# Kernel tuning notes

Hardware: AMD Instinct MI355X
Metric: run time of the kernel (lower is better)

## Reference

```python
import jax, jax.numpy as jnp
import numpy as np

B, S, E = 2, 1024, 768
H, D = 12, 64          # num_heads, head_dim
M = 768                # mlp_hidden_size
Q = 4                  # q_stride
EPS = 1e-5


def _layernorm(x, w, b):
    mu = x.mean(-1, keepdims=True)
    var = ((x - mu) ** 2).mean(-1, keepdims=True)
    return (x - mu) * jax.lax.rsqrt(var + EPS) * w + b


def setup_inputs() -> dict:
    key = jax.random.key(0)
    ks = jax.random.split(key, 16)
    s = 0.02
    d = {
        'x': jax.random.normal(ks[0], (B, S, E), jnp.float32),
        'ln1_w': jnp.ones((E,), jnp.float32), 'ln1_b': jnp.zeros((E,), jnp.float32),
        'Wq': jax.random.normal(ks[1], (E, E), jnp.float32) * s, 'bq': jnp.zeros((E,), jnp.float32),
        'Wk': jax.random.normal(ks[2], (E, E), jnp.float32) * s, 'bk': jnp.zeros((E,), jnp.float32),
        'Wv': jax.random.normal(ks[3], (E, E), jnp.float32) * s, 'bv': jnp.zeros((E,), jnp.float32),
        'Wo': jax.random.normal(ks[4], (E, E), jnp.float32) * s, 'bo': jnp.zeros((E,), jnp.float32),
        'pond': jnp.zeros((), jnp.float32),  # ponderation_param
        'ln2_w': jnp.ones((E,), jnp.float32), 'ln2_b': jnp.zeros((E,), jnp.float32),
        'fc1_W': jax.random.normal(ks[5], (Q * M, E), jnp.float32) * s, 'fc1_b': jnp.zeros((Q * M,), jnp.float32),
        'vqc_W': jax.random.normal(ks[6], (M, M), jnp.float32) * s, 'vqc_b': jnp.zeros((M,), jnp.float32),
        'fc2_W': jax.random.normal(ks[7], (E, Q * M), jnp.float32) * s, 'fc2_b': jnp.zeros((E,), jnp.float32),
    }
    return d


def reference(x, ln1_w, ln1_b, Wq, bq, Wk, bk, Wv, bv, Wo, bo, pond,
              ln2_w, ln2_b, fc1_W, fc1_b, vqc_W, vqc_b, fc2_W, fc2_b):
    # --- attention sublayer ---
    h = _layernorm(x, ln1_w, ln1_b)
    def heads(W, b):
        return (h @ W.T + b).reshape(B, S, H, D).transpose(0, 2, 1, 3)  # [B,H,S,D]
    q, k, v = heads(Wq, bq), heads(Wk, bk), heads(Wv, bv)

    # N=2: einsum with identity A reduces to q k^T
    logits = jnp.einsum('bhid,bhjd->bhij', q, k) / jnp.sqrt(jnp.float32(D))
    attn = jax.nn.softmax(logits, axis=-1)  # dropout is identity at inference

    # RBF similarity blending ('linear' ponderation)
    q_norm = (q ** 2).sum(-1, keepdims=True)                  # [B,H,S,1]
    k_norm = (k ** 2).sum(-1, keepdims=True).swapaxes(-2, -1)  # [B,H,1,S]
    d2 = jnp.maximum(q_norm + k_norm - 2.0 * jnp.einsum('bhid,bhjd->bhij', q, k), 0.0)
    sigma2 = jnp.clip(q_norm, 1e-8, 1e4)
    rbf = jnp.exp(-d2 / sigma2)
    rbf = rbf / jnp.maximum(rbf.sum(-1, keepdims=True), 1e-8)
    rbf = jnp.nan_to_num(rbf, nan=0.0, posinf=0.0, neginf=0.0)
    s_val = jax.nn.sigmoid(pond)
    p0, p1 = 1.0 - s_val, s_val
    attn = (p0 * attn + p1 * rbf) / (p0 + p1 + 1e-7)

    vals = jnp.einsum('bhij,bhjd->bhid', attn, v)
    vals = vals.transpose(0, 2, 1, 3).reshape(B, S, E)
    x = x + (vals @ Wo.T + bo)

    # --- sliced MLP sublayer (q_stride=4, overlapping offset-1 slices) ---
    y = _layernorm(x, ln2_w, ln2_b)
    h1 = y @ fc1_W.T + fc1_b                                  # [B,S,Q*M]
    slices = jnp.stack([h1[:, :, i:i + M] for i in range(Q)], axis=2)  # [B,S,Q,M]
    z = slices @ vqc_W.T + vqc_b                              # vqc (linear fallback)
    z = z.transpose(0, 1, 3, 2).reshape(B, S, Q * M)          # permute(0,1,3,2).view
    z = jax.nn.gelu(z, approximate=False)
    out = z @ fc2_W.T + fc2_b
    return x + out
```

## Files before the change

### kernel.cpp

```cpp
#include <hip/hip_runtime.h>
#include <math.h>

#define E_DIM 768
#define S_LEN 1024
#define B_SZ 2
#define H_CNT 12
#define D_HEAD 64
#define M_DIM 768
#define Q_STRIDE 4
#define N_FC1 771

typedef __attribute__((ext_vector_type(8))) short bf16x8;
typedef __attribute__((ext_vector_type(4))) float f32x4;

#define AS1 __attribute__((address_space(1)))
#define AS3 __attribute__((address_space(3)))

__device__ __forceinline__ void gld_lds16(void* lds, const void* g) {
    __builtin_amdgcn_global_load_lds((const AS1 void*)g, (AS3 void*)lds, 16, 0, 0);
}

__device__ __forceinline__ short f2bf(float f) {
    unsigned u = __float_as_uint(f);
    unsigned r = (u + 0x7fffu + ((u >> 16) & 1u)) >> 16;
    return (short)r;
}

__device__ __forceinline__ float bf2f(short s) {
    return __uint_as_float(((unsigned)(unsigned short)s) << 16);
}


__device__ __forceinline__ float block_reduce_sum(float v, volatile float* red) {
#pragma unroll
    for (int off = 32; off > 0; off >>= 1) v += __shfl_xor(v, off);
    __syncthreads();
    if ((threadIdx.x & 63) == 0) red[threadIdx.x >> 6] = v;
    __syncthreads();
    return red[0] + red[1] + red[2] + red[3];
}


__global__ __launch_bounds__(256) void preamble(
        const float* __restrict__ Wq, const float* __restrict__ Wk,
        const float* __restrict__ Wv, const float* __restrict__ Wo,
        const float* __restrict__ fc1W, const float* __restrict__ vqcW,
        const float* __restrict__ fc2W, short* __restrict__ dst,
        const float* __restrict__ bq, const float* __restrict__ bk,
        const float* __restrict__ bv, float* __restrict__ bqkv,
        const float* __restrict__ x, const float* __restrict__ ln1_w,
        const float* __restrict__ ln1_b, short* __restrict__ actb) {
    __shared__ float red[4];
    int tid = threadIdx.x;
    if (blockIdx.x < 2048) {
        int row = blockIdx.x;
        const float* xr = x + (size_t)row * E_DIM;
        float v0 = xr[tid], v1 = xr[tid + 256], v2 = xr[tid + 512];
        float s = block_reduce_sum(v0 + v1 + v2, red);
        float mu = s * (1.0f / E_DIM);
        float d0 = v0 - mu, d1 = v1 - mu, d2 = v2 - mu;
        float var = block_reduce_sum(d0 * d0 + d1 * d1 + d2 * d2, red) * (1.0f / E_DIM);
        float rs = rsqrtf(var + 1e-5f);
        short* orow = actb + (size_t)row * E_DIM;
        orow[tid]       = f2bf(d0 * rs * ln1_w[tid]       + ln1_b[tid]);
        orow[tid + 256] = f2bf(d1 * rs * ln1_w[tid + 256] + ln1_b[tid + 256]);
        orow[tid + 512] = f2bf(d2 * rs * ln1_w[tid + 512] + ln1_b[tid + 512]);
        return;
    }
    if (blockIdx.x == 2048) {
#pragma unroll
        for (int u = 0; u < 9; u++) {
            int i = tid + u * 256;
            float v = (i < 768) ? bq[i] : (i < 1536) ? bk[i - 768] : bv[i - 1536];
            bqkv[i] = v;
        }
        return;
    }
    int t = (blockIdx.x - 2049) * 256 + tid;
    if (t >= 1475136) return;
    int e = t * 4;
    const float* src; int off;
    if      (e < 589824)  { src = Wq;   off = e; }
    else if (e < 1179648) { src = Wk;   off = e - 589824; }
    else if (e < 1769472) { src = Wv;   off = e - 1179648; }
    else if (e < 2359296) { src = Wo;   off = e - 1769472; }
    else if (e < 2951424) { src = fc1W; off = e - 2359296; }
    else if (e < 3541248) { src = vqcW; off = e - 2951424; }
    else                  { src = fc2W; off = e - 3541248; }
    float4 v = *(const float4*)(src + off);
    short4 o = make_short4(f2bf(v.x), f2bf(v.y), f2bf(v.z), f2bf(v.w));
    *(short4*)(dst + e) = o;
}


template <int OUTMODE, int MR>
__global__ __launch_bounds__(256, 2) void gemm_bf16(
        const short* __restrict__ A, int lda,
        const short* __restrict__ W, int ldw,
        const float* __restrict__ bias,
        void* __restrict__ outp, int ldo, size_t spitch,
        short* __restrict__ Kfp, short* __restrict__ Vfp,
        int N, int klen, int dogelu) {
    constexpr int MI = MR / 32;
    constexpr int AH = MR * 32;
    constexpr int NA = MR / 64;
    constexpr int ASL = 2 * AH;
    __shared__ short At[2 * ASL];
    __shared__ short Bt[2 * 8192];
    const int tid = threadIdx.x;
    const int lane = tid & 63;
    const int wave = tid >> 6;
    const int wr = (wave >> 1) * (MI * 16);
    const int wc = (wave & 1) * 64;
    const int ml = lane & 15;
    const int kq = lane >> 4;
    const int row0 = blockIdx.y * MR;
    const int col0 = blockIdx.x * 128;
    const int kbase = blockIdx.z * klen;

    const short* Ag[NA]; int aoff[NA];
#pragma unroll
    for (int u = 0; u < NA; u++) {
        int c = tid + u * 256;
        int am = c >> 2, ak = ((c & 3) ^ ((am >> 1) & 3)) * 8;
        Ag[u] = A + (size_t)(row0 + am) * lda + ak + kbase;
        aoff[u] = c * 8;
    }
    const int c0 = tid, c1 = tid + 256;
    const int bm0 = c0 >> 2, bk0 = (((c0 & 3) ^ ((bm0 >> 1) & 3))) * 8;
    const int bm1 = c1 >> 2, bk1 = (((c1 & 3) ^ ((bm1 >> 1) & 3))) * 8;
    int wrow0 = col0 + bm0; if (wrow0 > N - 1) wrow0 = N - 1;
    int wrow1 = col0 + bm1; if (wrow1 > N - 1) wrow1 = N - 1;
    const short* Wg0 = W + (size_t)wrow0 * ldw + bk0 + kbase;
    const short* Wg1 = W + (size_t)wrow1 * ldw + bk1 + kbase;

    const int kxor = (kq ^ ((ml >> 1) & 3)) * 8;

    f32x4 acc[MI][4];
#pragma unroll
    for (int i = 0; i < MI; i++)
#pragma unroll
        for (int j = 0; j < 4; j++) acc[i][j] = {0.f, 0.f, 0.f, 0.f};

    auto stage = [&](int buf, int k0) {
        short* Ab = At + buf * ASL;
        short* Bb = Bt + buf * 8192;
#pragma unroll
        for (int u = 0; u < NA; u++) {
            gld_lds16(Ab + aoff[u], Ag[u] + k0);
            gld_lds16(Ab + AH + aoff[u], Ag[u] + k0 + 32);
        }
        gld_lds16(Bb + c0 * 8, Wg0 + k0);
        gld_lds16(Bb + c1 * 8, Wg1 + k0);
        gld_lds16(Bb + 4096 + c0 * 8, Wg0 + k0 + 32);
        gld_lds16(Bb + 4096 + c1 * 8, Wg1 + k0 + 32);
    };

    stage(0, 0);
    int cur = 0;
    for (int k0 = 0; k0 < klen; k0 += 64) {
        __syncthreads();
        if (k0 + 64 < klen) stage(cur ^ 1, k0 + 64);
        const short* Ac = At + cur * ASL;
        const short* Bc = Bt + cur * 8192;
#pragma unroll
        for (int half = 0; half < 2; half++) {
            const short* Ah = Ac + half * AH;
            const short* Bh = Bc + half * 4096;
            bf16x8 af[MI], bfr[4];
#pragma unroll
            for (int i = 0; i < MI; i++)
                af[i] = *(const bf16x8*)&Ah[(wr + i * 16 + ml) * 32 + kxor];
#pragma unroll
            for (int j = 0; j < 4; j++)
                bfr[j] = *(const bf16x8*)&Bh[(wc + j * 16 + ml) * 32 + kxor];
#pragma unroll
            for (int i = 0; i < MI; i++)
#pragma unroll
                for (int j = 0; j < 4; j++)
                    acc[i][j] = __builtin_amdgcn_mfma_f32_16x16x32_bf16(af[i], bfr[j], acc[i][j], 0, 0, 0);
        }
        cur ^= 1;
    }

#pragma unroll
    for (int i = 0; i < MI; i++) {
#pragma unroll
        for (int j = 0; j < 4; j++) {
#pragma unroll
            for (int rr = 0; rr < 4; rr++) {
                int r = row0 + wr + i * 16 + kq * 4 + rr;
                int c = col0 + wc + j * 16 + ml;
                if (c < N) {
                    float v = acc[i][j][rr];
                    if (OUTMODE < 4) v += bias[c];
                    if (OUTMODE == 2 && dogelu)
                        v = 0.5f * v * (1.0f + erff(v * 0.70710678118654752f));
                    if (OUTMODE == 2) {
                        ((short*)outp)[(size_t)(r >> 2) * ldo + c * 4 + (r & 3)] = f2bf(v);
                    } else if (OUTMODE == 5) {
                        ((short*)outp)[blockIdx.z * spitch + (size_t)r * ldo + c] = f2bf(v);
                    } else if (OUTMODE == 3) {
                        int s = r & 1023, bb = r >> 10;
                        if (c < 768) {
                            ((short*)outp)[(size_t)r * 768 + c] = f2bf(v);
                        } else if (c < 1536) {
                            int df = c - 768; int hh = df >> 6, d = df & 63;
                            int bh2 = bb * 12 + hh;
                            size_t idx = ((size_t)(bh2 * 64 + (s >> 4)) * 2 + (d >> 5)) * 512
                                       + (size_t)((d >> 3) & 3) * 128 + (size_t)(s & 15) * 8 + (d & 7);
                            Kfp[idx] = f2bf(v);
                        } else {
                            int df = c - 1536; int hh = df >> 6, d = df & 63;
                            int bh2 = bb * 12 + hh;
                            size_t idx = ((size_t)(bh2 * 32 + (s >> 5))) * 2048
                                       + (size_t)(d >> 4) * 512 + (size_t)((s >> 3) & 3) * 128
                                       + (size_t)(d & 15) * 8 + (s & 7);
                            Vfp[idx] = f2bf(v);
                        }
                    }
                }
            }
        }
    }
}


__global__ __launch_bounds__(256) void reduce_wo_ln(
        const short* __restrict__ part, const float* __restrict__ bo,
        const float* __restrict__ x, const float* __restrict__ w,
        const float* __restrict__ bvec, float* __restrict__ x2,
        short* __restrict__ y) {
    __shared__ float red[4];
    int row = blockIdx.x, tid = threadIdx.x;
    const size_t SP = (size_t)2048 * 768;
    const short* pr = part + (size_t)row * 768;
    const float* xr = x + (size_t)row * 768;
    float* x2r = x2 + (size_t)row * 768;
    float v[3];
#pragma unroll
    for (int u = 0; u < 3; u++) {
        int c = tid + u * 256;
        float s = bo[c] + xr[c];
#pragma unroll
        for (int z = 0; z < 4; z++) s += bf2f(pr[z * SP + c]);
        v[u] = s; x2r[c] = s;
    }
    float s = block_reduce_sum(v[0] + v[1] + v[2], red);
    float mu = s * (1.0f / 768.f);
    float d0 = v[0] - mu, d1 = v[1] - mu, d2 = v[2] - mu;
    float var = block_reduce_sum(d0 * d0 + d1 * d1 + d2 * d2, red) * (1.0f / 768.f);
    float rs = rsqrtf(var + 1e-5f);
    short* orow = y + (size_t)row * 768;
    orow[tid]       = f2bf(d0 * rs * w[tid]       + bvec[tid]);
    orow[tid + 256] = f2bf(d1 * rs * w[tid + 256] + bvec[tid + 256]);
    orow[tid + 512] = f2bf(d2 * rs * w[tid + 512] + bvec[tid + 512]);
}

__global__ __launch_bounds__(256) void reduce_fc1_expand(
        const short* __restrict__ part, const float* __restrict__ b,
        const short* __restrict__ y, const short* __restrict__ w768,
        short* __restrict__ Avqc) {
    __shared__ float row[772];
    __shared__ float red[4];
    int r = blockIdx.x, tid = threadIdx.x;
    const size_t SP = (size_t)2048 * 768;
    const short* pr = part + (size_t)r * 768;
#pragma unroll
    for (int u = 0; u < 3; u++) {
        int c = tid + u * 256;
        float s = b[c];
#pragma unroll
        for (int z = 0; z < 4; z++) s += bf2f(pr[z * SP + c]);
        row[c] = s;
    }
    const short* yr = y + (size_t)r * 768;
    float y0 = bf2f(yr[tid]), y1 = bf2f(yr[tid + 256]), y2 = bf2f(yr[tid + 512]);
#pragma unroll
    for (int k = 0; k < 3; k++) {
        const short* wk = w768 + k * 768;
        float s = y0 * bf2f(wk[tid]) + y1 * bf2f(wk[tid + 256]) + y2 * bf2f(wk[tid + 512]);
        s = block_reduce_sum(s, red);
        if (tid == 0) row[768 + k] = s + b[768 + k];
    }
    __syncthreads();
#pragma unroll
    for (int q = 0; q < 4; q++) {
        short* orow = Avqc + (size_t)(r * 4 + q) * 768;
#pragma unroll
        for (int u = 0; u < 3; u++) {
            int m = tid + u * 256;
            orow[m] = f2bf(row[m + q]);
        }
    }
}

__global__ __launch_bounds__(256) void reduce_fc2(
        const short* __restrict__ part, const float* __restrict__ b,
        const float* __restrict__ x2, float* __restrict__ out) {
    int t = blockIdx.x * 256 + threadIdx.x;
    int row = t / 192;
    int c = (t - row * 192) * 4;
    size_t off = (size_t)row * 768 + c;
    const size_t SP = (size_t)2048 * 768;
    float4 bb = *(const float4*)(b + c);
    float4 xx = *(const float4*)(x2 + off);
    float o0 = bb.x + xx.x, o1 = bb.y + xx.y, o2 = bb.z + xx.z, o3 = bb.w + xx.w;
#pragma unroll
    for (int z = 0; z < 4; z++) {
        short4 v = *(const short4*)(part + z * SP + off);
        o0 += bf2f(v.x); o1 += bf2f(v.y); o2 += bf2f(v.z); o3 += bf2f(v.w);
    }
    float4 o = make_float4(o0, o1, o2, o3);
    *(float4*)(out + off) = o;
}


__global__ __launch_bounds__(256) void attn_mfma(
        const short* __restrict__ Qb,
        const short* __restrict__ Kf,
        const short* __restrict__ Vf,
        const float* __restrict__ pond,
        short* __restrict__ vals) {
    __shared__ __align__(16) short Kt[2 * 4096];
    __shared__ __align__(16) short Vt[2 * 4096];
    __shared__ float qn_l[4][16];
    __shared__ float is_l[4][16];
    __shared__ float esx[2][16], rsx[2][16];
    __shared__ __align__(16) short Pe[4 * 16 * 72];
    __shared__ __align__(16) short Pr[4 * 16 * 72];

    const int tid = threadIdx.x;
    const int lane = tid & 63;
    const int wave = tid >> 6;
    const int wq = wave & 1;
    const int wp = wave >> 1;
    const int ml = lane & 15;
    const int kq = lane >> 4;
    const int qt2 = blockIdx.x, h = blockIdx.y, b = blockIdx.z;
    const int bh = b * H_CNT + h;

    const int qrow = b * S_LEN + qt2 * 32 + wq * 16 + ml;
    const short* qp = Qb + (size_t)qrow * 768 + h * 64 + kq * 8;
    bf16x8 aq0 = *(const bf16x8*)qp;
    bf16x8 aq1 = *(const bf16x8*)(qp + 32);

    float qn_part = 0.f;
#pragma unroll
    for (int e = 0; e < 8; e++) {
        float v0 = bf2f(aq0[e]), v1 = bf2f(aq1[e]);
        qn_part += v0 * v0 + v1 * v1;
    }
    qn_part += __shfl_xor(qn_part, 16);
    qn_part += __shfl_xor(qn_part, 32);
    if (kq == 0) {
        qn_l[wave][ml] = qn_part;
        float sig = fminf(fmaxf(qn_part, 1e-8f), 1e4f);
        is_l[wave][ml] = 1.0f / sig;
    }
    __syncthreads();

    float qn_r[4], is_r[4];
#pragma unroll
    for (int r = 0; r < 4; r++) {
        qn_r[r] = qn_l[wave][kq * 4 + r];
        is_r[r] = is_l[wave][kq * 4 + r];
    }

    f32x4 Oe[4], Or[4];
#pragma unroll
    for (int dt = 0; dt < 4; dt++) { Oe[dt] = {0.f,0.f,0.f,0.f}; Or[dt] = {0.f,0.f,0.f,0.f}; }
    float es_p[4] = {0.f,0.f,0.f,0.f}, rs_p[4] = {0.f,0.f,0.f,0.f};

    const short* KfB = Kf + (size_t)bh * 65536;
    const short* VfB = Vf + (size_t)bh * 65536;
    short* PeW = Pe + wave * 1152;
    short* PrW = Pr + wave * 1152;
    const short* KtW = Kt + wp * 4096;
    const short* VtW = Vt + wp * 4096;

    for (int it = 0; it < 8; it++) {
        __syncthreads();
        {
            const short* sk0 = KfB + it * 4096 + tid * 8;
            gld_lds16(Kt + tid * 8, sk0);
            gld_lds16(Kt + 2048 + tid * 8, sk0 + 2048);
            const short* sk1 = KfB + (it + 8) * 4096 + tid * 8;
            gld_lds16(Kt + 4096 + tid * 8, sk1);
            gld_lds16(Kt + 6144 + tid * 8, sk1 + 2048);
            const short* sv0 = VfB + it * 4096 + tid * 8;
            gld_lds16(Vt + tid * 8, sv0);
            gld_lds16(Vt + 2048 + tid * 8, sv0 + 2048);
            const short* sv1 = VfB + (it + 8) * 4096 + tid * 8;
            gld_lds16(Vt + 4096 + tid * 8, sv1);
            gld_lds16(Vt + 6144 + tid * 8, sv1 + 2048);
        }
        __syncthreads();

#pragma unroll
        for (int jtl = 0; jtl < 4; jtl++) {
            bf16x8 bk0 = *(const bf16x8*)&KtW[(jtl * 2 + 0) * 512 + lane * 8];
            bf16x8 bk1 = *(const bf16x8*)&KtW[(jtl * 2 + 1) * 512 + lane * 8];
            float knp = 0.f;
#pragma unroll
            for (int e = 0; e < 8; e++) {
                float k0v = bf2f(bk0[e]), k1v = bf2f(bk1[e]);
                knp += k0v * k0v + k1v * k1v;
            }
            knp += __shfl_xor(knp, 16);
            knp += __shfl_xor(knp, 32);
            f32x4 c = {0.f,0.f,0.f,0.f};
            c = __builtin_amdgcn_mfma_f32_16x16x32_bf16(aq0, bk0, c, 0, 0, 0);
            c = __builtin_amdgcn_mfma_f32_16x16x32_bf16(aq1, bk1, c, 0, 0, 0);
#pragma unroll
            for (int r = 0; r < 4; r++) {
                float qk = c[r];
                float e = __expf(qk * 0.125f);
                float tt = (2.f * qk - qn_r[r] - knp) * is_r[r];
                float rb = fminf(__expf(tt), 1.0f);
                es_p[r] += e; rs_p[r] += rb;
                PeW[(kq * 4 + r) * 72 + jtl * 16 + ml] = f2bf(e);
                PrW[(kq * 4 + r) * 72 + jtl * 16 + ml] = f2bf(rb);
            }
        }

#pragma unroll
        for (int jcl = 0; jcl < 2; jcl++) {
            bf16x8 pa_e = *(const bf16x8*)&PeW[ml * 72 + jcl * 32 + kq * 8];
            bf16x8 pa_r = *(const bf16x8*)&PrW[ml * 72 + jcl * 32 + kq * 8];
#pragma unroll
            for (int dt = 0; dt < 4; dt++) {
                bf16x8 bv = *(const bf16x8*)&VtW[(jcl * 4 + dt) * 512 + lane * 8];
                Oe[dt] = __builtin_amdgcn_mfma_f32_16x16x32_bf16(pa_e, bv, Oe[dt], 0, 0, 0);
                Or[dt] = __builtin_amdgcn_mfma_f32_16x16x32_bf16(pa_r, bv, Or[dt], 0, 0, 0);
            }
        }
    }

#pragma unroll
    for (int off = 1; off <= 8; off <<= 1) {
#pragma unroll
        for (int r = 0; r < 4; r++) {
            es_p[r] += __shfl_xor(es_p[r], off);
            rs_p[r] += __shfl_xor(rs_p[r], off);
        }
    }

    __syncthreads();
    float* cb = (float*)Kt;
    if (wp == 1) {
        float* cl = cb + (size_t)(wq * 64 + lane) * 32;
#pragma unroll
        for (int dt = 0; dt < 4; dt++)
#pragma unroll
            for (int r = 0; r < 4; r++) {
                cl[dt * 4 + r] = Oe[dt][r];
                cl[16 + dt * 4 + r] = Or[dt][r];
            }
        if (ml == 0) {
#pragma unroll
            for (int r = 0; r < 4; r++) {
                esx[wq][kq * 4 + r] = es_p[r];
                rsx[wq][kq * 4 + r] = rs_p[r];
            }
        }
    }
    __syncthreads();
    if (wp == 0) {
        float p = pond[0];
        float sv = 1.0f / (1.0f + __expf(-p));
        float p0 = 1.0f - sv, p1 = sv;
        float blendinv = 1.0f / (p0 + p1 + 1e-7f);
        const float* cl = cb + (size_t)(wq * 64 + lane) * 32;
        float we[4], wr[4];
#pragma unroll
        for (int r = 0; r < 4; r++) {
            float es = es_p[r] + esx[wq][kq * 4 + r];
            float rs = rs_p[r] + rsx[wq][kq * 4 + r];
            we[r] = p0 * blendinv / es;
            wr[r] = p1 * blendinv / fmaxf(rs, 1e-8f);
        }
#pragma unroll
        for (int dt = 0; dt < 4; dt++) {
#pragma unroll
            for (int r = 0; r < 4; r++) {
                float oe = Oe[dt][r] + cl[dt * 4 + r];
                float orr = Or[dt][r] + cl[16 + dt * 4 + r];
                float v = oe * we[r] + orr * wr[r];
                int token = b * S_LEN + qt2 * 32 + wq * 16 + kq * 4 + r;
                vals[(size_t)token * 768 + h * 64 + dt * 16 + ml] = f2bf(v);
            }
        }
    }
}


extern "C" void kernel_launch(void* const* d_in, const int* in_sizes, int n_in,
                              void* d_out, int out_size, void* d_ws, size_t ws_size,
                              hipStream_t stream) {
    const float* x     = (const float*)d_in[0];
    const float* ln1_w = (const float*)d_in[1];
    const float* ln1_b = (const float*)d_in[2];
    const float* Wq    = (const float*)d_in[3];
    const float* bq    = (const float*)d_in[4];
    const float* Wk    = (const float*)d_in[5];
    const float* bk    = (const float*)d_in[6];
    const float* Wv    = (const float*)d_in[7];
    const float* bv    = (const float*)d_in[8];
    const float* Wo    = (const float*)d_in[9];
    const float* bo    = (const float*)d_in[10];
    const float* pond  = (const float*)d_in[11];
    const float* ln2_w = (const float*)d_in[12];
    const float* ln2_b = (const float*)d_in[13];
    const float* fc1_W = (const float*)d_in[14];
    const float* fc1_b = (const float*)d_in[15];
    const float* vqc_W = (const float*)d_in[16];
    const float* vqc_b = (const float*)d_in[17];
    const float* fc2_W = (const float*)d_in[18];
    const float* fc2_b = (const float*)d_in[19];
    float* out = (float*)d_out;

    char* p = (char*)d_ws;
    short* Qb   = (short*)p;  p += (size_t)2048 * 768 * 2;
    short* Kfb  = (short*)p;  p += (size_t)2048 * 768 * 2;
    short* Vfb  = (short*)p;  p += (size_t)2048 * 768 * 2;
    float* x2   = (float*)p;  p += (size_t)2048 * 768 * 4;
    float* bqkv = (float*)p;  p += 2304 * 4;
    short* actb = (short*)p;  p += (size_t)2048 * 768 * 2;
    short* g    = (short*)p;  p += (size_t)2048 * 3072 * 2;
    short* Avqc = (short*)p;  p += (size_t)8192 * 768 * 2;
    short* partb = (short*)p; p += (size_t)4 * 2048 * 768 * 2;
    short* wreg = (short*)p;  p += (size_t)5900544 * 2;
    short* Wqkvb = wreg;
    short* Wob   = wreg + 1769472;
    short* fc1b  = wreg + 2359296;
    short* vqcb  = wreg + 2951424;
    short* fc2b  = wreg + 3541248;

    dim3 blk(256);
    const size_t SP = (size_t)2048 * 768;

    preamble<<<7812, blk, 0, stream>>>(Wq, Wk, Wv, Wo, fc1_W, vqc_W, fc2_W, wreg,
                                       bq, bk, bv, bqkv, x, ln1_w, ln1_b, actb);
    gemm_bf16<3, 64><<<dim3(18, 32, 1), blk, 0, stream>>>(actb, 768, Wqkvb, 768, bqkv,
                                                          Qb, 768, 0, Kfb, Vfb, 2304, 768, 0);
    attn_mfma<<<dim3(32, 12, 2), blk, 0, stream>>>(Qb, Kfb, Vfb, pond, actb);
    gemm_bf16<5, 64><<<dim3(6, 32, 4), blk, 0, stream>>>(actb, 768, Wob, 768, nullptr,
                                                         partb, 768, SP,
                                                         nullptr, nullptr, 768, 192, 0);
    reduce_wo_ln<<<2048, blk, 0, stream>>>(partb, bo, x, ln2_w, ln2_b, x2, actb);
    gemm_bf16<5, 64><<<dim3(6, 32, 4), blk, 0, stream>>>(actb, 768, fc1b, 768, nullptr,
                                                         partb, 768, SP,
                                                         nullptr, nullptr, 768, 192, 0);
    reduce_fc1_expand<<<2048, blk, 0, stream>>>(partb, fc1_b, actb, fc1b + 768 * 768, Avqc);
    gemm_bf16<2, 64><<<dim3(6, 128, 1), blk, 0, stream>>>(Avqc, 768, vqcb, 768, vqc_b,
                                                          g, 3072, 0, nullptr, nullptr, 768, 768, 1);
    gemm_bf16<5, 64><<<dim3(6, 32, 4), blk, 0, stream>>>(g, 3072, fc2b, 3072, nullptr,
                                                         partb, 768, SP,
                                                         nullptr, nullptr, 768, 768, 0);
    reduce_fc2<<<1536, blk, 0, stream>>>(partb, fc2_b, x2, out);
}
```

Baseline: 151.7 us.

## Read attention K/V directly from global memory and remap blocks per XCD

The attention kernel no longer stages K and V tiles into LDS through global_load_lds with two barriers per iteration. Each wave now loads its MFMA operands straight from global memory and relies on L2 reuse. The 3D grid becomes a 1D grid whose block index is remapped so that blocks sharing a (batch, head) land on the same XCD, which should improve L2 locality. LDS use shrinks to a single combined P buffer, and launch bounds request 4 blocks per CU for higher occupancy. The trade-off is that global load latency is now exposed directly in the inner loop with no explicit prefetch.

```diff
diff --git a/kernel.cpp b/kernel.cpp
--- a/kernel.cpp
+++ b/kernel.cpp
@@ -316,19 +316,16 @@
 }
 
 
-__global__ __launch_bounds__(256) void attn_mfma(
+__global__ __launch_bounds__(256, 4) void attn_mfma(
         const short* __restrict__ Qb,
         const short* __restrict__ Kf,
         const short* __restrict__ Vf,
         const float* __restrict__ pond,
         short* __restrict__ vals) {
-    __shared__ __align__(16) short Kt[2 * 4096];
-    __shared__ __align__(16) short Vt[2 * 4096];
+    __shared__ __align__(16) short Pbuf[2 * 4 * 16 * 72];
     __shared__ float qn_l[4][16];
     __shared__ float is_l[4][16];
     __shared__ float esx[2][16], rsx[2][16];
-    __shared__ __align__(16) short Pe[4 * 16 * 72];
-    __shared__ __align__(16) short Pr[4 * 16 * 72];
 
     const int tid = threadIdx.x;
     const int lane = tid & 63;
@@ -337,8 +334,13 @@
     const int wp = wave >> 1;
     const int ml = lane & 15;
     const int kq = lane >> 4;
-    const int qt2 = blockIdx.x, h = blockIdx.y, b = blockIdx.z;
-    const int bh = b * H_CNT + h;
+
+    const int fid = blockIdx.x;
+    const int w = (fid & 7) * 96 + (fid >> 3);
+    const int qt2 = w & 31;
+    const int bh = w >> 5;
+    const int b = (bh >= 12) ? 1 : 0;
+    const int h = bh - b * 12;
 
     const int qrow = b * S_LEN + qt2 * 32 + wq * 16 + ml;
     const short* qp = Qb + (size_t)qrow * 768 + h * 64 + kq * 8;
@@ -374,33 +376,17 @@
 
     const short* KfB = Kf + (size_t)bh * 65536;
     const short* VfB = Vf + (size_t)bh * 65536;
-    short* PeW = Pe + wave * 1152;
-    short* PrW = Pr + wave * 1152;
-    const short* KtW = Kt + wp * 4096;
-    const short* VtW = Vt + wp * 4096;
+    short* PeW = Pbuf + wave * 1152;
+    short* PrW = Pbuf + 4608 + wave * 1152;
 
     for (int it = 0; it < 8; it++) {
-        __syncthreads();
-        {
-            const short* sk0 = KfB + it * 4096 + tid * 8;
-            gld_lds16(Kt + tid * 8, sk0);
-            gld_lds16(Kt + 2048 + tid * 8, sk0 + 2048);
-            const short* sk1 = KfB + (it + 8) * 4096 + tid * 8;
-            gld_lds16(Kt + 4096 + tid * 8, sk1);
-            gld_lds16(Kt + 6144 + tid * 8, sk1 + 2048);
-            const short* sv0 = VfB + it * 4096 + tid * 8;
-            gld_lds16(Vt + tid * 8, sv0);
-            gld_lds16(Vt + 2048 + tid * 8, sv0 + 2048);
-            const short* sv1 = VfB + (it + 8) * 4096 + tid * 8;
-            gld_lds16(Vt + 4096 + tid * 8, sv1);
-            gld_lds16(Vt + 6144 + tid * 8, sv1 + 2048);
-        }
-        __syncthreads();
+        const short* Kit = KfB + (size_t)(it + 8 * wp) * 4096;
+        const short* Vit = VfB + (size_t)(it + 8 * wp) * 4096;
 
 #pragma unroll
         for (int jtl = 0; jtl < 4; jtl++) {
-            bf16x8 bk0 = *(const bf16x8*)&KtW[(jtl * 2 + 0) * 512 + lane * 8];
-            bf16x8 bk1 = *(const bf16x8*)&KtW[(jtl * 2 + 1) * 512 + lane * 8];
+            bf16x8 bk0 = *(const bf16x8*)&Kit[(jtl * 2 + 0) * 512 + lane * 8];
+            bf16x8 bk1 = *(const bf16x8*)&Kit[(jtl * 2 + 1) * 512 + lane * 8];
             float knp = 0.f;
 #pragma unroll
             for (int e = 0; e < 8; e++) {
@@ -430,7 +416,7 @@
             bf16x8 pa_r = *(const bf16x8*)&PrW[ml * 72 + jcl * 32 + kq * 8];
 #pragma unroll
             for (int dt = 0; dt < 4; dt++) {
-                bf16x8 bv = *(const bf16x8*)&VtW[(jcl * 4 + dt) * 512 + lane * 8];
+                bf16x8 bv = *(const bf16x8*)&Vit[(jcl * 4 + dt) * 512 + lane * 8];
                 Oe[dt] = __builtin_amdgcn_mfma_f32_16x16x32_bf16(pa_e, bv, Oe[dt], 0, 0, 0);
                 Or[dt] = __builtin_amdgcn_mfma_f32_16x16x32_bf16(pa_r, bv, Or[dt], 0, 0, 0);
             }
@@ -447,7 +433,7 @@
     }
 
     __syncthreads();
-    float* cb = (float*)Kt;
+    float* cb = (float*)Pbuf;
     if (wp == 1) {
         float* cl = cb + (size_t)(wq * 64 + lane) * 32;
 #pragma unroll
@@ -544,7 +530,7 @@
                                        bq, bk, bv, bqkv, x, ln1_w, ln1_b, actb);
     gemm_bf16<3, 64><<<dim3(18, 32, 1), blk, 0, stream>>>(actb, 768, Wqkvb, 768, bqkv,
                                                           Qb, 768, 0, Kfb, Vfb, 2304, 768, 0);
-    attn_mfma<<<dim3(32, 12, 2), blk, 0, stream>>>(Qb, Kfb, Vfb, pond, actb);
+    attn_mfma<<<768, blk, 0, stream>>>(Qb, Kfb, Vfb, pond, actb);
     gemm_bf16<5, 64><<<dim3(6, 32, 4), blk, 0, stream>>>(actb, 768, Wob, 768, nullptr,
                                                          partb, 768, SP,
                                                          nullptr, nullptr, 768, 192, 0);
```

Result: slower. 159.6 us (+5.2%).

## Compute q/k squared norms in QKV GEMM epilogue and remap attention grid

Applied to the files above, without the earlier changes.

The QKV projection GEMM now accumulates per-row squared norms of each Q and K head in its epilogue, reduces them across lanes and writes them to small global buffers. The attention kernel reads these instead of recomputing the query norm and the key norm for every key tile, so it drops the per-tile bf16 unpack, square and shuffle work. The norms now come from fp32 values before bf16 rounding rather than from the rounded values. The attention launch also becomes a 1D grid of 768 blocks with a swizzled mapping that interleaves (batch, head, q-tile) across blocks, likely to spread work and improve cache locality.

```diff
diff --git a/kernel.cpp b/kernel.cpp
--- a/kernel.cpp
+++ b/kernel.cpp
@@ -100,7 +100,8 @@
         const float* __restrict__ bias,
         void* __restrict__ outp, int ldo, size_t spitch,
         short* __restrict__ Kfp, short* __restrict__ Vfp,
-        int N, int klen, int dogelu) {
+        int N, int klen, int dogelu,
+        float* __restrict__ qnG, float* __restrict__ knG) {
     constexpr int MI = MR / 32;
     constexpr int AH = MR * 32;
     constexpr int NA = MR / 64;
@@ -183,6 +184,13 @@
         cur ^= 1;
     }
 
+    float sq[MI][4];
+    if constexpr (OUTMODE == 3) {
+#pragma unroll
+        for (int i = 0; i < MI; i++)
+#pragma unroll
+            for (int rr = 0; rr < 4; rr++) sq[i][rr] = 0.f;
+    }
 #pragma unroll
     for (int i = 0; i < MI; i++) {
 #pragma unroll
@@ -201,6 +209,7 @@
                     } else if (OUTMODE == 5) {
                         ((short*)outp)[blockIdx.z * spitch + (size_t)r * ldo + c] = f2bf(v);
                     } else if (OUTMODE == 3) {
+                        sq[i][rr] += v * v;
                         int s = r & 1023, bb = r >> 10;
                         if (c < 768) {
                             ((short*)outp)[(size_t)r * 768 + c] = f2bf(v);
@@ -223,6 +232,30 @@
             }
         }
     }
+
+    if constexpr (OUTMODE == 3) {
+        int cb = col0 + wc;
+        if (cb < 1536) {
+            float* dst = (cb < 768) ? qnG : knG;
+            int hh = ((cb < 768) ? cb : cb - 768) >> 6;
+#pragma unroll
+            for (int i = 0; i < MI; i++) {
+#pragma unroll
+                for (int rr = 0; rr < 4; rr++) {
+                    float s = sq[i][rr];
+                    s += __shfl_xor(s, 1);
+                    s += __shfl_xor(s, 2);
+                    s += __shfl_xor(s, 4);
+                    s += __shfl_xor(s, 8);
+                    if (ml == 0) {
+                        int r = row0 + wr + i * 16 + kq * 4 + rr;
+                        int bb = r >> 10, sidx = r & 1023;
+                        dst[(size_t)(bb * 12 + hh) * 1024 + sidx] = s;
+                    }
+                }
+            }
+        }
+    }
 }
 
 
@@ -321,11 +354,11 @@
         const short* __restrict__ Kf,
         const short* __restrict__ Vf,
         const float* __restrict__ pond,
+        const float* __restrict__ qnG,
+        const float* __restrict__ knG,
         short* __restrict__ vals) {
     __shared__ __align__(16) short Kt[2 * 4096];
     __shared__ __align__(16) short Vt[2 * 4096];
-    __shared__ float qn_l[4][16];
-    __shared__ float is_l[4][16];
     __shared__ float esx[2][16], rsx[2][16];
     __shared__ __align__(16) short Pe[4 * 16 * 72];
     __shared__ __align__(16) short Pr[4 * 16 * 72];
@@ -337,35 +370,27 @@
     const int wp = wave >> 1;
     const int ml = lane & 15;
     const int kq = lane >> 4;
-    const int qt2 = blockIdx.x, h = blockIdx.y, b = blockIdx.z;
-    const int bh = b * H_CNT + h;
+
+    const int fid = blockIdx.x;
+    const int w = (fid & 7) * 96 + (fid >> 3);
+    const int qt2 = w & 31;
+    const int bh = w >> 5;
+    const int b = (bh >= 12) ? 1 : 0;
+    const int h = bh - b * 12;
 
     const int qrow = b * S_LEN + qt2 * 32 + wq * 16 + ml;
     const short* qp = Qb + (size_t)qrow * 768 + h * 64 + kq * 8;
     bf16x8 aq0 = *(const bf16x8*)qp;
     bf16x8 aq1 = *(const bf16x8*)(qp + 32);
 
-    float qn_part = 0.f;
-#pragma unroll
-    for (int e = 0; e < 8; e++) {
-        float v0 = bf2f(aq0[e]), v1 = bf2f(aq1[e]);
-        qn_part += v0 * v0 + v1 * v1;
-    }
-    qn_part += __shfl_xor(qn_part, 16);
-    qn_part += __shfl_xor(qn_part, 32);
-    if (kq == 0) {
-        qn_l[wave][ml] = qn_part;
-        float sig = fminf(fmaxf(qn_part, 1e-8f), 1e4f);
-        is_l[wave][ml] = 1.0f / sig;
-    }
-    __syncthreads();
-
+    const float* qnB = qnG + (size_t)bh * 1024 + qt2 * 32 + wq * 16;
     float qn_r[4], is_r[4];
 #pragma unroll
     for (int r = 0; r < 4; r++) {
-        qn_r[r] = qn_l[wave][kq * 4 + r];
-        is_r[r] = is_l[wave][kq * 4 + r];
-    }
+        qn_r[r] = qnB[kq * 4 + r];
+        is_r[r] = 1.0f / fminf(fmaxf(qn_r[r], 1e-8f), 1e4f);
+    }
+    const float* knB = knG + (size_t)bh * 1024;
 
     f32x4 Oe[4], Or[4];
 #pragma unroll
@@ -395,20 +420,18 @@
             gld_lds16(Vt + 4096 + tid * 8, sv1);
             gld_lds16(Vt + 6144 + tid * 8, sv1 + 2048);
         }
+        float knt[4];
+        {
+            const float* knI = knB + (it + 8 * wp) * 64 + ml;
+#pragma unroll
+            for (int jtl = 0; jtl < 4; jtl++) knt[jtl] = knI[jtl * 16];
+        }
         __syncthreads();
 
 #pragma unroll
         for (int jtl = 0; jtl < 4; jtl++) {
             bf16x8 bk0 = *(const bf16x8*)&KtW[(jtl * 2 + 0) * 512 + lane * 8];
             bf16x8 bk1 = *(const bf16x8*)&KtW[(jtl * 2 + 1) * 512 + lane * 8];
-            float knp = 0.f;
-#pragma unroll
-            for (int e = 0; e < 8; e++) {
-                float k0v = bf2f(bk0[e]), k1v = bf2f(bk1[e]);
-                knp += k0v * k0v + k1v * k1v;
-            }
-            knp += __shfl_xor(knp, 16);
-            knp += __shfl_xor(knp, 32);
             f32x4 c = {0.f,0.f,0.f,0.f};
             c = __builtin_amdgcn_mfma_f32_16x16x32_bf16(aq0, bk0, c, 0, 0, 0);
             c = __builtin_amdgcn_mfma_f32_16x16x32_bf16(aq1, bk1, c, 0, 0, 0);
@@ -416,7 +439,7 @@
             for (int r = 0; r < 4; r++) {
                 float qk = c[r];
                 float e = __expf(qk * 0.125f);
-                float tt = (2.f * qk - qn_r[r] - knp) * is_r[r];
+                float tt = (2.f * qk - qn_r[r] - knt[jtl]) * is_r[r];
                 float rb = fminf(__expf(tt), 1.0f);
                 es_p[r] += e; rs_p[r] += rb;
                 PeW[(kq * 4 + r) * 72 + jtl * 16 + ml] = f2bf(e);
@@ -526,6 +549,8 @@
     short* Vfb  = (short*)p;  p += (size_t)2048 * 768 * 2;
     float* x2   = (float*)p;  p += (size_t)2048 * 768 * 4;
     float* bqkv = (float*)p;  p += 2304 * 4;
+    float* qnG  = (float*)p;  p += (size_t)24 * 1024 * 4;
+    float* knG  = (float*)p;  p += (size_t)24 * 1024 * 4;
     short* actb = (short*)p;  p += (size_t)2048 * 768 * 2;
     short* g    = (short*)p;  p += (size_t)2048 * 3072 * 2;
     short* Avqc = (short*)p;  p += (size_t)8192 * 768 * 2;
@@ -543,20 +568,25 @@
     preamble<<<7812, blk, 0, stream>>>(Wq, Wk, Wv, Wo, fc1_W, vqc_W, fc2_W, wreg,
                                        bq, bk, bv, bqkv, x, ln1_w, ln1_b, actb);
     gemm_bf16<3, 64><<<dim3(18, 32, 1), blk, 0, stream>>>(actb, 768, Wqkvb, 768, bqkv,
-                                                          Qb, 768, 0, Kfb, Vfb, 2304, 768, 0);
-    attn_mfma<<<dim3(32, 12, 2), blk, 0, stream>>>(Qb, Kfb, Vfb, pond, actb);
+                                                          Qb, 768, 0, Kfb, Vfb, 2304, 768, 0,
+                                                          qnG, knG);
+    attn_mfma<<<768, blk, 0, stream>>>(Qb, Kfb, Vfb, pond, qnG, knG, actb);
     gemm_bf16<5, 64><<<dim3(6, 32, 4), blk, 0, stream>>>(actb, 768, Wob, 768, nullptr,
                                                          partb, 768, SP,
-                                                         nullptr, nullptr, 768, 192, 0);
+                                                         nullptr, nullptr, 768, 192, 0,
+                                                         nullptr, nullptr);
     reduce_wo_ln<<<2048, blk, 0, stream>>>(partb, bo, x, ln2_w, ln2_b, x2, actb);
     gemm_bf16<5, 64><<<dim3(6, 32, 4), blk, 0, stream>>>(actb, 768, fc1b, 768, nullptr,
                                                          partb, 768, SP,
-                                                         nullptr, nullptr, 768, 192, 0);
+                                                         nullptr, nullptr, 768, 192, 0,
+                                                         nullptr, nullptr);
     reduce_fc1_expand<<<2048, blk, 0, stream>>>(partb, fc1_b, actb, fc1b + 768 * 768, Avqc);
     gemm_bf16<2, 64><<<dim3(6, 128, 1), blk, 0, stream>>>(Avqc, 768, vqcb, 768, vqc_b,
-                                                          g, 3072, 0, nullptr, nullptr, 768, 768, 1);
+                                                          g, 3072, 0, nullptr, nullptr, 768, 768, 1,
+                                                          nullptr, nullptr);
     gemm_bf16<5, 64><<<dim3(6, 32, 4), blk, 0, stream>>>(g, 3072, fc2b, 3072, nullptr,
                                                          partb, 768, SP,
-                                                         nullptr, nullptr, 768, 768, 0);
+                                                         nullptr, nullptr, 768, 768, 0,
+                                                         nullptr, nullptr);
     reduce_fc2<<<1536, blk, 0, stream>>>(partb, fc2_b, x2, out);
 }
```

Result: no change. 150.3 us (-0.9%).
